# Kernel tuning notes

Measured on AMD Instinct MI355X. Metric: run time of the kernel, lower is better.

Reference implementation:

```python
import jax, jax.numpy as jnp
import numpy as np

N_ITER = 30  # bisection iterations for entmax-1.5 threshold


def segment_entmax15(x, seg, num_segments):
    """Entmax alpha=1.5 over variable-size segments (the DGL mailbox dim).
    p_i = [ (alpha-1)*x_i - tau ]_+ ** (1/(alpha-1)), sum_segment p = 1.
    Threshold tau found by bisection per segment (monotone decreasing sum).
    """
    X = 0.5 * x  # (alpha-1) * x
    m = jax.ops.segment_max(X, seg, num_segments=num_segments)

    def body(i, bounds):
        lo, hi = bounds
        tau = 0.5 * (lo + hi)
        p = jnp.square(jnp.maximum(X - tau[seg], 0.0))
        s = jax.ops.segment_sum(p, seg, num_segments=num_segments)
        lo = jnp.where(s > 1.0, tau, lo)
        hi = jnp.where(s > 1.0, hi, tau)
        return (lo, hi)

    lo, hi = jax.lax.fori_loop(0, N_ITER, body, (m - 1.0, m))
    tau = 0.5 * (lo + hi)
    p = jnp.square(jnp.maximum(X - tau[seg], 0.0))
    denom = jax.ops.segment_sum(p, seg, num_segments=num_segments)
    return p / jnp.maximum(denom, 1e-12)[seg]


def setup_inputs() -> dict:
    key = jax.random.key(0)
    k1, k2, k3, k4, k5, k6 = jax.random.split(key, 6)
    N, E = 100000, 3200000
    in_dim, out_dim, num_community = 128, 64, 32
    h = jax.random.normal(k1, (N, in_dim), dtype=jnp.float32)
    u = jax.random.normal(k2, (N, num_community), dtype=jnp.float32)
    src = jax.random.randint(k3, (E,), 0, N, dtype=jnp.int32)
    dst = jax.random.randint(k4, (E,), 0, N, dtype=jnp.int32)
    Wfc = jax.random.normal(k5, (out_dim, in_dim), dtype=jnp.float32) * (1.0 / np.sqrt(in_dim))
    W2 = jax.random.normal(k6, (1, 2 * num_community), dtype=jnp.float32) * (1.0 / np.sqrt(2 * num_community))
    return {"h": h, "u": u, "src": src, "dst": dst, "Wfc": Wfc, "W2": W2}


def reference(h, u, src, dst, Wfc, W2):
    N = h.shape[0]
    # node transform: z = fc(h)
    z = h @ Wfc.T  # [N, out_dim]
    # edge attention: a = attn_fc2(cat(u_src, u_dst)); entmax over dim=1 of
    # a [E,1] tensor is over a singleton axis -> identically 1.0
    z2 = jnp.concatenate([u[src], u[dst]], axis=1)  # [E, 2*num_community]
    a = z2 @ W2.T  # [E, 1]
    e = jnp.ones_like(a)[:, 0]  # entmax-1.5 over singleton dim == 1
    # reduce: alpha = entmax15 over each destination node's mailbox of e
    alpha = segment_entmax15(e, dst, N)  # [E]
    # h_v = sum_{e->v} alpha_e * z_src(e) * e_e
    contrib = (alpha * e)[:, None] * z[src]  # [E, out_dim]
    h_out = jax.ops.segment_sum(contrib, dst, num_segments=N)
    return h_out
```

## Files before the change

### kernel.cpp

```cpp
#include <hip/hip_runtime.h>
#include <hip/hip_fp16.h>


#define WS_ALIGN(x) (((x) + (size_t)255) & ~(size_t)255)
#define BBITS 6
#define BNODES 64
#define CAP 4096
#define MAXBUCK 2048
#define TILE 32768

__device__ inline unsigned pack_h2(float a, float b) {
    __half2 h = __floats2half2_rn(a, b);
    return *reinterpret_cast<unsigned*>(&h);
}

__global__ __launch_bounds__(512) void bucket_count(const int* __restrict__ dst,
                                                    int* __restrict__ bcnt,
                                                    int* __restrict__ hists,
                                                    int E, int nbuck) {
    __shared__ int h[MAXBUCK];
    for (int i = threadIdx.x; i < nbuck; i += 512) h[i] = 0;
    __syncthreads();
    int base = blockIdx.x * TILE;
    for (int k = 0; k < TILE / 512; k++) {
        int e = base + threadIdx.x + k * 512;
        if (e < E) atomicAdd(&h[dst[e] >> BBITS], 1);
    }
    __syncthreads();
    int* hrow = hists + (size_t)blockIdx.x * nbuck;
    for (int i = threadIdx.x; i < nbuck; i += 512) {
        int v = h[i];
        hrow[i] = v;
        if (v) atomicAdd(&bcnt[i], v);
    }
}

__global__ __launch_bounds__(1024) void scan_buckets(const int* __restrict__ bcnt,
                                                     int* __restrict__ bases,
                                                     int E, int nbuck) {
    __shared__ int sp[1024];
    int t = threadIdx.x;
    int a = (2 * t < nbuck) ? bcnt[2 * t] : 0;
    int b = (2 * t + 1 < nbuck) ? bcnt[2 * t + 1] : 0;
    sp[t] = a + b;
    __syncthreads();
    for (int off = 1; off < 1024; off <<= 1) {
        int x = (t >= off) ? sp[t - off] : 0;
        __syncthreads();
        sp[t] += x;
        __syncthreads();
    }
    int ex = sp[t] - (a + b);
    if (2 * t < nbuck)     bases[2 * t] = ex;
    if (2 * t + 1 < nbuck) bases[2 * t + 1] = ex + a;
    if (t == 0) bases[nbuck] = E;
}

__global__ __launch_bounds__(256) void scan_hists(int* __restrict__ hists,
                                                  const int* __restrict__ bases,
                                                  int nblk, int nbuck) {
    int b = blockIdx.x * 256 + threadIdx.x;
    if (b >= nbuck) return;
    int run = bases[b];
    int k = 0;
    for (; k + 8 <= nblk; k += 8) {
        int v[8];
        size_t i0 = (size_t)k * nbuck + b;
#pragma unroll
        for (int j = 0; j < 8; j++) v[j] = hists[i0 + (size_t)j * nbuck];
#pragma unroll
        for (int j = 0; j < 8; j++) {
            hists[i0 + (size_t)j * nbuck] = run;
            run += v[j];
        }
    }
    for (; k < nblk; k++) {
        size_t i = (size_t)k * nbuck + b;
        int v = hists[i];
        hists[i] = run; run += v;
    }
}

__global__ __launch_bounds__(512) void bin_scatter(const int* __restrict__ src,
                                                   const int* __restrict__ dst,
                                                   const int* __restrict__ hists,
                                                   unsigned* __restrict__ binned,
                                                   int E, int nbuck) {
    __shared__ int gbase[MAXBUCK], cnt2[MAXBUCK];
    const int* hrow = hists + (size_t)blockIdx.x * nbuck;
    for (int i = threadIdx.x; i < nbuck; i += 512) {
        gbase[i] = hrow[i];
        cnt2[i] = 0;
    }
    __syncthreads();
    int base = blockIdx.x * TILE;
    for (int k = 0; k < TILE / 512; k++) {
        int e = base + threadIdx.x + k * 512;
        if (e < E) {
            int d = dst[e];
            int b = d >> BBITS;
            int lo = atomicAdd(&cnt2[b], 1);
            binned[gbase[b] + lo] = ((unsigned)(d & (BNODES - 1)) << 17) |
                                    (unsigned)src[e];
        }
    }
}

__global__ __launch_bounds__(256) void gemm_z(const float* __restrict__ h,
                                              const float* __restrict__ W,
                                              __half* __restrict__ z, int N) {
    __shared__ float Wl[64 * 128];
    for (int j = threadIdx.x; j < 2048; j += 256) {
        reinterpret_cast<float4*>(Wl)[j] = reinterpret_cast<const float4*>(W)[j];
    }
    __syncthreads();
    int row = blockIdx.x * 256 + threadIdx.x;
    if (row >= N) return;
    float acc[64];
#pragma unroll
    for (int c = 0; c < 64; c++) acc[c] = 0.f;
    const float4* hr = reinterpret_cast<const float4*>(&h[(size_t)row * 128]);
    for (int kv = 0; kv < 32; kv++) {
        float4 hv = hr[kv];
#pragma unroll
        for (int c = 0; c < 64; c++) {
            float4 wv = *reinterpret_cast<const float4*>(&Wl[c * 128 + kv * 4]);
            acc[c] += hv.x * wv.x + hv.y * wv.y + hv.z * wv.z + hv.w * wv.w;
        }
    }
    uint4* zr = reinterpret_cast<uint4*>(&z[(size_t)row * 64]);
#pragma unroll
    for (int c = 0; c < 8; c++) {
        uint4 pk;
        pk.x = pack_h2(acc[8 * c + 0], acc[8 * c + 1]);
        pk.y = pack_h2(acc[8 * c + 2], acc[8 * c + 3]);
        pk.z = pack_h2(acc[8 * c + 4], acc[8 * c + 5]);
        pk.w = pack_h2(acc[8 * c + 6], acc[8 * c + 7]);
        zr[c] = pk;
    }
}

__global__ __launch_bounds__(1024, 8) void bucket_gather(
        const unsigned* __restrict__ binned,
        const int* __restrict__ bases,
        const __half* __restrict__ z,
        float* __restrict__ out, int N) {
    __shared__ unsigned sed[CAP];
    __shared__ int hist[BNODES];
    __shared__ int ioff[BNODES];
    __shared__ int eoff[BNODES];
    __shared__ int curs[BNODES];
    __shared__ int degl[BNODES];

    int b = blockIdx.x;
    int s0 = bases[b], s1 = bases[b + 1];
    int tid = threadIdx.x;
    int wid = tid >> 6, lane = tid & 63;

    if (tid < BNODES) degl[tid] = 0;

    float acc[4];
#pragma unroll
    for (int s = 0; s < 4; s++) acc[s] = 0.f;

    for (int c0 = s0; c0 < s1; c0 += CAP) {
        int cnt = s1 - c0;
        if (cnt > CAP) cnt = CAP;
        if (tid < BNODES) hist[tid] = 0;
        __syncthreads();
        for (int i = tid; i < cnt; i += 1024) {
            unsigned p = binned[c0 + i];
            atomicAdd(&hist[(p >> 17) & (BNODES - 1)], 1);
        }
        __syncthreads();
        if (tid < 64) {
            int v = hist[tid];
            int inc = v;
#pragma unroll
            for (int off = 1; off < 64; off <<= 1) {
                int x = __shfl_up(inc, off);
                if (tid >= off) inc += x;
            }
            ioff[tid] = inc;
            eoff[tid] = inc - v;
            curs[tid] = inc - v;
            degl[tid] += v;
        }
        __syncthreads();
        for (int i = tid; i < cnt; i += 1024) {
            unsigned p = binned[c0 + i];
            int ld = (p >> 17) & (BNODES - 1);
            int pos = atomicAdd(&curs[ld], 1);
            sed[pos] = p & 0x1FFFFu;
        }
        __syncthreads();
#pragma unroll
        for (int s = 0; s < 4; s++) {
            int r = wid * 4 + s;
            int e0 = eoff[r], e1 = ioff[r];
            float f0 = 0.f, f1 = 0.f, f2 = 0.f, f3 = 0.f;
            float f4 = 0.f, f5 = 0.f, f6 = 0.f, f7 = 0.f;
            int e = e0;
            for (; e + 8 <= e1; e += 8) {
                int q0 = sed[e],     q1 = sed[e + 1], q2 = sed[e + 2], q3 = sed[e + 3];
                int q4 = sed[e + 4], q5 = sed[e + 5], q6 = sed[e + 6], q7 = sed[e + 7];
                f0 += __half2float(z[(size_t)q0 * 64 + lane]);
                f1 += __half2float(z[(size_t)q1 * 64 + lane]);
                f2 += __half2float(z[(size_t)q2 * 64 + lane]);
                f3 += __half2float(z[(size_t)q3 * 64 + lane]);
                f4 += __half2float(z[(size_t)q4 * 64 + lane]);
                f5 += __half2float(z[(size_t)q5 * 64 + lane]);
                f6 += __half2float(z[(size_t)q6 * 64 + lane]);
                f7 += __half2float(z[(size_t)q7 * 64 + lane]);
            }
            for (; e < e1; e++)
                f0 += __half2float(z[(size_t)sed[e] * 64 + lane]);
            acc[s] += ((f0 + f1) + (f2 + f3)) + ((f4 + f5) + (f6 + f7));
        }
        __syncthreads();
    }
    int node0 = b << BBITS;
#pragma unroll
    for (int s = 0; s < 4; s++) {
        int node = node0 + wid * 4 + s;
        if (node < N) {
            int d = degl[wid * 4 + s];
            float sc = (d > 0) ? 1.0f / (float)d : 0.f;
            out[(size_t)node * 64 + lane] = acc[s] * sc;
        }
    }
}

__global__ __launch_bounds__(256) void count_deg(const int* __restrict__ dst,
                                                 int* __restrict__ cnt, int E) {
    int e = blockIdx.x * 256 + threadIdx.x;
    if (e < E) atomicAdd(&cnt[dst[e]], 1);
}

__global__ __launch_bounds__(256) void edge_add(const __half* __restrict__ z,
                                                const int* __restrict__ src,
                                                const int* __restrict__ dst,
                                                float* __restrict__ out, int E) {
    int e = blockIdx.x * 4 + (threadIdx.x >> 6);
    int lane = threadIdx.x & 63;
    if (e >= E) return;
    int s = src[e];
    int d = dst[e];
    float v = __half2float(z[(size_t)s * 64 + lane]);
    atomicAdd(&out[(size_t)d * 64 + lane], v);
}

__global__ __launch_bounds__(256) void scale_out(float* __restrict__ out,
                                                 const int* __restrict__ deg, int N) {
    int v = blockIdx.x * 4 + (threadIdx.x >> 6);
    int lane = threadIdx.x & 63;
    if (v >= N) return;
    int d = deg[v];
    if (d > 0) out[(size_t)v * 64 + lane] *= (1.0f / (float)d);
}

extern "C" void kernel_launch(void* const* d_in, const int* in_sizes, int n_in,
                              void* d_out, int out_size, void* d_ws, size_t ws_size,
                              hipStream_t stream) {
    const float* h   = (const float*)d_in[0];
    const int*   src = (const int*)d_in[2];
    const int*   dst = (const int*)d_in[3];
    const float* Wfc = (const float*)d_in[4];
    float*       out = (float*)d_out;

    int N = in_sizes[0] / 128;
    int E = in_sizes[2];
    (void)n_in;

    int nbuck = (N + BNODES - 1) >> BBITS;
    int nwgE  = (E + TILE - 1) / TILE;

    size_t sz_z    = WS_ALIGN((size_t)N * 64 * sizeof(__half));
    size_t sz_bin  = WS_ALIGN((size_t)E * sizeof(unsigned));
    size_t sz_bkt  = WS_ALIGN((size_t)(2 * MAXBUCK + 2) * sizeof(int));
    size_t need_fast = sz_z + sz_bin + sz_bkt;
    size_t need_hists = (size_t)nwgE * nbuck * sizeof(int);

    char*     ws     = (char*)d_ws;
    __half*   z      = (__half*)ws;
    unsigned* binned = (unsigned*)(ws + sz_z);
    int*      bcnt   = (int*)(ws + sz_z + sz_bin);
    int*      bases  = bcnt + MAXBUCK;

    int* hists = (int*)d_out;

    bool can_fast = (N <= (1 << 17)) && (nbuck <= MAXBUCK) &&
                    (ws_size >= need_fast) &&
                    ((size_t)out_size * sizeof(float) >= need_hists);

    if (can_fast) {
        hipMemsetAsync(bcnt, 0, (size_t)nbuck * sizeof(int), stream);
        bucket_count<<<nwgE, 512, 0, stream>>>(dst, bcnt, hists, E, nbuck);
        scan_buckets<<<1, 1024, 0, stream>>>(bcnt, bases, E, nbuck);
        scan_hists<<<(nbuck + 255) / 256, 256, 0, stream>>>(hists, bases, nwgE, nbuck);
        bin_scatter<<<nwgE, 512, 0, stream>>>(src, dst, hists, binned, E, nbuck);
        gemm_z<<<(N + 255) / 256, 256, 0, stream>>>(h, Wfc, z, N);
        bucket_gather<<<nbuck, 1024, 0, stream>>>(binned, bases, z, out, N);
    } else if (ws_size >= sz_z + WS_ALIGN((size_t)N * sizeof(int))) {
        int* deg = (int*)(ws + sz_z);
        hipMemsetAsync(deg, 0, (size_t)N * sizeof(int), stream);
        hipMemsetAsync(out, 0, (size_t)N * 64 * sizeof(float), stream);
        count_deg<<<(E + 255) / 256, 256, 0, stream>>>(dst, deg, E);
        gemm_z<<<(N + 255) / 256, 256, 0, stream>>>(h, Wfc, z, N);
        edge_add<<<(E + 3) / 4, 256, 0, stream>>>(z, src, dst, out, E);
        scale_out<<<(N + 3) / 4, 256, 0, stream>>>(out, deg, N);
    }
}
```

Before: 256.5 us.

## Stage edges in LDS by bucket before coalesced scatter to binned array

bin_scatter now counts a local histogram per tile, scans it in shared memory, and sorts edges into LDS by bucket, then writes them to global memory contiguously per bucket. The global writes become more coalesced instead of scattered 4-byte stores. TILE drops from 32768 to 8192 and blocks shrink to 256 threads so the staging fits in LDS, which quadruples the number of blocks and the size of the hists array. It also re-reads dst in a second pass.

Result: no change. 253.5 us (median of 2 runs) (-1.2%).

```diff
diff --git a/kernel.cpp b/kernel.cpp
--- a/kernel.cpp
+++ b/kernel.cpp
@@ -7,28 +7,28 @@
 #define BNODES 64
 #define CAP 4096
 #define MAXBUCK 2048
-#define TILE 32768
+#define TILE 8192
 
 __device__ inline unsigned pack_h2(float a, float b) {
     __half2 h = __floats2half2_rn(a, b);
     return *reinterpret_cast<unsigned*>(&h);
 }
 
-__global__ __launch_bounds__(512) void bucket_count(const int* __restrict__ dst,
+__global__ __launch_bounds__(256) void bucket_count(const int* __restrict__ dst,
                                                     int* __restrict__ bcnt,
                                                     int* __restrict__ hists,
                                                     int E, int nbuck) {
     __shared__ int h[MAXBUCK];
-    for (int i = threadIdx.x; i < nbuck; i += 512) h[i] = 0;
+    for (int i = threadIdx.x; i < nbuck; i += 256) h[i] = 0;
     __syncthreads();
     int base = blockIdx.x * TILE;
-    for (int k = 0; k < TILE / 512; k++) {
-        int e = base + threadIdx.x + k * 512;
+    for (int k = 0; k < TILE / 256; k++) {
+        int e = base + threadIdx.x + k * 256;
         if (e < E) atomicAdd(&h[dst[e] >> BBITS], 1);
     }
     __syncthreads();
     int* hrow = hists + (size_t)blockIdx.x * nbuck;
-    for (int i = threadIdx.x; i < nbuck; i += 512) {
+    for (int i = threadIdx.x; i < nbuck; i += 256) {
         int v = h[i];
         hrow[i] = v;
         if (v) atomicAdd(&bcnt[i], v);
@@ -81,27 +81,80 @@
     }
 }
 
-__global__ __launch_bounds__(512) void bin_scatter(const int* __restrict__ src,
+__global__ __launch_bounds__(256) void bin_scatter(const int* __restrict__ src,
                                                    const int* __restrict__ dst,
                                                    const int* __restrict__ hists,
                                                    unsigned* __restrict__ binned,
                                                    int E, int nbuck) {
-    __shared__ int gbase[MAXBUCK], cnt2[MAXBUCK];
+    __shared__ unsigned sed[TILE];
+    __shared__ unsigned short sbuck[TILE];
+    __shared__ int lofs[MAXBUCK];
+    __shared__ int lcur[MAXBUCK];
+    __shared__ int gb[MAXBUCK];
+    __shared__ int wsum[4];
+
+    int tid = threadIdx.x;
     const int* hrow = hists + (size_t)blockIdx.x * nbuck;
-    for (int i = threadIdx.x; i < nbuck; i += 512) {
-        gbase[i] = hrow[i];
-        cnt2[i] = 0;
+    for (int i = tid; i < nbuck; i += 256) {
+        lofs[i] = 0;
+        gb[i] = hrow[i];
     }
     __syncthreads();
     int base = blockIdx.x * TILE;
-    for (int k = 0; k < TILE / 512; k++) {
-        int e = base + threadIdx.x + k * 512;
-        if (e < E) {
-            int d = dst[e];
+    int lim = E - base;
+    if (lim > TILE) lim = TILE;
+    for (int k = 0; k < TILE / 256; k++) {
+        int i = tid + k * 256;
+        if (i < lim) atomicAdd(&lofs[dst[base + i] >> BBITS], 1);
+    }
+    __syncthreads();
+    {
+        int v[8];
+        int i0 = tid * 8;
+        int s = 0;
+#pragma unroll
+        for (int j = 0; j < 8; j++) {
+            int i = i0 + j;
+            v[j] = (i < nbuck) ? lofs[i] : 0;
+            s += v[j];
+        }
+        int lane = tid & 63, wid = tid >> 6;
+        int inc = s;
+#pragma unroll
+        for (int off = 1; off < 64; off <<= 1) {
+            int x = __shfl_up(inc, off);
+            if (lane >= off) inc += x;
+        }
+        if (lane == 63) wsum[wid] = inc;
+        __syncthreads();
+        int carry = 0;
+        for (int j = 0; j < wid; j++) carry += wsum[j];
+        int run = inc - s + carry;
+#pragma unroll
+        for (int j = 0; j < 8; j++) {
+            int i = i0 + j;
+            if (i < nbuck) { lofs[i] = run; lcur[i] = run; }
+            run += v[j];
+        }
+    }
+    __syncthreads();
+    for (int k = 0; k < TILE / 256; k++) {
+        int i = tid + k * 256;
+        if (i < lim) {
+            int d = dst[base + i];
             int b = d >> BBITS;
-            int lo = atomicAdd(&cnt2[b], 1);
-            binned[gbase[b] + lo] = ((unsigned)(d & (BNODES - 1)) << 17) |
-                                    (unsigned)src[e];
+            int pos = atomicAdd(&lcur[b], 1);
+            sed[pos] = ((unsigned)(d & (BNODES - 1)) << 17) |
+                       (unsigned)src[base + i];
+            sbuck[pos] = (unsigned short)b;
+        }
+    }
+    __syncthreads();
+    for (int k = 0; k < TILE / 256; k++) {
+        int i = tid + k * 256;
+        if (i < lim) {
+            int b = sbuck[i];
+            binned[gb[b] + (i - lofs[b])] = sed[i];
         }
     }
 }
@@ -295,10 +348,10 @@
 
     if (can_fast) {
         hipMemsetAsync(bcnt, 0, (size_t)nbuck * sizeof(int), stream);
-        bucket_count<<<nwgE, 512, 0, stream>>>(dst, bcnt, hists, E, nbuck);
+        bucket_count<<<nwgE, 256, 0, stream>>>(dst, bcnt, hists, E, nbuck);
         scan_buckets<<<1, 1024, 0, stream>>>(bcnt, bases, E, nbuck);
         scan_hists<<<(nbuck + 255) / 256, 256, 0, stream>>>(hists, bases, nwgE, nbuck);
-        bin_scatter<<<nwgE, 512, 0, stream>>>(src, dst, hists, binned, E, nbuck);
+        bin_scatter<<<nwgE, 256, 0, stream>>>(src, dst, hists, binned, E, nbuck);
         gemm_z<<<(N + 255) / 256, 256, 0, stream>>>(h, Wfc, z, N);
         bucket_gather<<<nbuck, 1024, 0, stream>>>(binned, bases, z, out, N);
     } else if (ws_size >= sz_z + WS_ALIGN((size_t)N * sizeof(int))) {
```
